# Performance work log

Hardware: AMD Instinct MI355X
Metric: run time of the kernel (lower is better)

Reference implementation:

```python
import jax, jax.numpy as jnp
import numpy as np

EPS = 1.1920929e-07  # torch nn.RMSNorm default eps = finfo(float32).eps
COS_EPS = 1e-8       # torch F.cosine_similarity denominator clamp

def rms_norm(x):
    # nn.RMSNorm(head_dim, elementwise_affine=False)
    return x / jnp.sqrt(jnp.mean(x * x, axis=-1, keepdims=True) + EPS)

def slerp(low, high, val):
    # spherical interpolation per last dim
    cos = jnp.sum(low * high, -1) / jnp.maximum(
        jnp.linalg.norm(low, axis=-1) * jnp.linalg.norm(high, axis=-1), COS_EPS)
    omega = jnp.arccos(jnp.clip(cos, -1.0 + 1e-7, 1.0 - 1e-7))[..., None]
    so = jnp.sin(omega)
    return (low * jnp.sin((1.0 - val) * omega) + high * jnp.sin(val * omega)) / so

def setup_inputs() -> dict:
    key = jax.random.key(0)
    k1, k2 = jax.random.split(key)
    z = jax.random.normal(k1, (8, 512, 2048), jnp.float32)          # [B, D, L]
    codebooks = rms_norm(jax.random.normal(k2, (8, 1024, 64), jnp.float32))  # [H, M, d]
    return {"z": z, "codebooks": codebooks}

def reference(z, codebooks, commitment_cost=0.25, decay=0.99):
    B, D, L = z.shape
    H, M, d = codebooks.shape
    # rearrange 'b (h d) l -> h (b l) d'
    z_split = z.reshape(B, H, d, L).transpose(1, 0, 3, 2).reshape(H, B * L, d)  # [H, N, d]

    sim = jnp.einsum('hnd,hmd->hnm', z_split, codebooks)          # [H, N, M]
    indices = jnp.argmax(sim, axis=-1)                            # [H, N]
    z_split_q = jnp.take_along_axis(codebooks, indices[:, :, None], axis=1)  # [H, N, d]

    commitment_loss = jnp.mean((jax.lax.stop_gradient(z_split) - z_split_q) ** 2)
    codebook_loss = jnp.mean((z_split - jax.lax.stop_gradient(z_split_q)) ** 2)
    vq_loss = codebook_loss + commitment_cost * commitment_loss

    # EMA slerp codebook update (training path, no_grad) -- vectorized over unique-code loop
    zs = jax.lax.stop_gradient(z_split)
    sums = jax.vmap(lambda zh, ih: jax.ops.segment_sum(zh, ih, num_segments=M))(zs, indices)  # [H, M, d]
    counts = jax.vmap(lambda ih: jax.ops.segment_sum(jnp.ones(ih.shape, zs.dtype), ih, num_segments=M))(indices)  # [H, M]
    means = sums / jnp.maximum(counts, 1.0)[..., None]
    updated = rms_norm(slerp(means, codebooks, decay))
    new_codebooks = jnp.where(counts[..., None] > 0, updated, codebooks)

    # rearrange back 'h (b l) d -> b (h d) l' and 'h (b l) -> b h l'
    z_q = z_split_q.reshape(H, B, L, d).transpose(1, 0, 3, 2).reshape(B, D, L)
    indices_out = indices.reshape(H, B, L).transpose(1, 0, 2)
    z_q = z + jax.lax.stop_gradient(z_q - z)  # straight-through
    return z_q, vq_loss, indices_out, new_codebooks
```

## Files before the change

kernel.cpp:

```cpp
#include <hip/hip_runtime.h>
#include <hip/hip_bf16.h>
#include <math.h>

#define BZ   8
#define DD   512
#define LL   2048
#define HH   8
#define MM   1024
#define DH   64
#define NN   (BZ * LL)
#define TOTAL_ELEMS (HH * NN * DH)

#define OFF_ZQ   0
#define OFF_LOSS 8388608
#define OFF_IDX  8388609
#define OFF_CB   8519681

#define CAP  128

#define WSB_SSE    0
#define WSB_CNT    64
#define WSB_LST    (64 + HH * MM * 4)
#define WSB_CBHI   (WSB_LST + HH * MM * CAP * 2)
#define WSB_CBLO   (WSB_CBHI + HH * MM * DH * 2)
#define WSB_ZS     (WSB_CBLO + HH * MM * DH * 2)
#define WS_NEED_BUCKET ((size_t)WSB_ZS + (size_t)HH * NN * DH * 4)

#define WS_PLANES_BYTE 64
#define WS_ZSPLIT_BYTE (64 + 2u * HH * MM * DH * 2)
#define WS_NEED_FAT    (WS_ZSPLIT_BYTE + (size_t)HH * NN * DH * 4)

typedef __attribute__((ext_vector_type(8))) short short8;
typedef __attribute__((ext_vector_type(4))) float float4v;

__device__ __forceinline__ unsigned short f2bf(float f) {
    unsigned int u = __builtin_bit_cast(unsigned int, f);
    u += 0x7FFFu + ((u >> 16) & 1u);
    return (unsigned short)(u >> 16);
}
__device__ __forceinline__ float bf2f(unsigned short s) {
    unsigned int u = ((unsigned int)s) << 16;
    return __builtin_bit_cast(float, u);
}

__device__ __forceinline__ void gload16(const short* g, short* l) {
    __builtin_amdgcn_global_load_lds(
        (const __attribute__((address_space(1))) unsigned int*)g,
        (__attribute__((address_space(3))) unsigned int*)l, 16, 0, 0);
}

__global__ __launch_bounds__(256) void cvt_cb_kernel(
    const float* __restrict__ cb, short* __restrict__ hip_, short* __restrict__ lop_)
{
    const int tid = blockIdx.x * 256 + threadIdx.x;
    const int c   = tid & 7;
    const int row = tid >> 3;
    const float* __restrict__ src = cb + (size_t)row * DH + c * 8;
    short hs[8], ls[8];
#pragma unroll
    for (int j = 0; j < 8; ++j) {
        const float f = src[j];
        const unsigned short hv = f2bf(f);
        hs[j] = (short)hv;
        ls[j] = (short)f2bf(f - bf2f(hv));
    }
    const int dst = row * DH + ((c ^ (row & 7)) * 8);
    *(short8*)&hip_[dst] = *(short8*)hs;
    *(short8*)&lop_[dst] = *(short8*)ls;
}

__global__ __launch_bounds__(512, 4) void vq_assign_kernel(
    const float* __restrict__ z,
    const float* __restrict__ cb,
    const short* __restrict__ cb_hi,
    const short* __restrict__ cb_lo,
    float* __restrict__ zq_out,
    float* __restrict__ idx_out,
    float* __restrict__ sse,
    float* __restrict__ zs,
    int*   __restrict__ cnts,
    unsigned short* __restrict__ lists)
{
    __shared__ __align__(16) short hi_lds[2][64 * DH];
    __shared__ __align__(16) short lo_lds[2][64 * DH];
    __shared__ float blk_err[8];

    const int t    = threadIdx.x;
    const int h    = blockIdx.y;
    const int lane = t & 63;
    const int g    = lane >> 4;
    const int nloc = lane & 15;
    const int w    = t >> 6;

    const int rbase = blockIdx.x * 256 + w * 32;

    short8 Bh0[2], Bh1[2], Bl0[2], Bl1[2];
#pragma unroll
    for (int u = 0; u < 2; ++u) {
        const int r = rbase + u * 16 + nloc;
        const int b = r >> 11;
        const int l = r & (LL - 1);
        const float* __restrict__ zbase = z + ((size_t)(b * DD + h * DH) * LL + l);
        float zv[16] __attribute__((aligned(16)));
#pragma unroll
        for (int j = 0; j < 8; ++j) zv[j]     = zbase[(size_t)(g * 8 + j) * LL];
#pragma unroll
        for (int j = 0; j < 8; ++j) zv[8 + j] = zbase[(size_t)(32 + g * 8 + j) * LL];

        if (zs) {
            float* __restrict__ zr_ = zs + ((size_t)h * NN + r) * DH;
            *(float4*)&zr_[g * 8]          = *(const float4*)&zv[0];
            *(float4*)&zr_[g * 8 + 4]      = *(const float4*)&zv[4];
            *(float4*)&zr_[32 + g * 8]     = *(const float4*)&zv[8];
            *(float4*)&zr_[32 + g * 8 + 4] = *(const float4*)&zv[12];
        }

        short bh[16], bl[16];
#pragma unroll
        for (int j = 0; j < 16; ++j) {
            const unsigned short hv = f2bf(zv[j]);
            bh[j] = (short)hv;
            bl[j] = (short)f2bf(zv[j] - bf2f(hv));
        }
        Bh0[u] = *(short8*)&bh[0];  Bh1[u] = *(short8*)&bh[8];
        Bl0[u] = *(short8*)&bl[0];  Bl1[u] = *(short8*)&bl[8];
    }

    const short* __restrict__ gh = cb_hi + (size_t)h * MM * DH;
    const short* __restrict__ gl = cb_lo + (size_t)h * MM * DH;

    auto stage = [&](int mt, int buf) {
        const short* sh = gh + (size_t)mt * 64 * DH;
        const short* sl = gl + (size_t)mt * 64 * DH;
        gload16(sh + t * 8, &hi_lds[buf][t * 8]);
        gload16(sl + t * 8, &lo_lds[buf][t * 8]);
    };

    stage(0, 0);

    float b1c[4], b2c[4];
    int   i1c[4], i2c[4];
#pragma unroll
    for (int c = 0; c < 4; ++c) { b1c[c] = -1e30f; b2c[c] = -1e30f; i1c[c] = 0; i2c[c] = 0; }

    const int sw8 = nloc & 7;

    for (int mt = 0; mt < MM / 64; ++mt) {
        __syncthreads();
        if (mt + 1 < MM / 64) stage(mt + 1, (mt + 1) & 1);
        const int buf = mt & 1;

#pragma unroll
        for (int s = 0; s < 4; ++s) {
            const short* hrow = &hi_lds[buf][(s * 16 + nloc) * DH];
            const short* lrow = &lo_lds[buf][(s * 16 + nloc) * DH];
            const short8 Ah0 = *(const short8*)&hrow[((g)     ^ sw8) * 8];
            const short8 Ah1 = *(const short8*)&hrow[((g + 4) ^ sw8) * 8];
            const short8 Al0 = *(const short8*)&lrow[((g)     ^ sw8) * 8];
            const short8 Al1 = *(const short8*)&lrow[((g + 4) ^ sw8) * 8];

            const int mbase = mt * 64 + s * 16 + g * 4;
#pragma unroll
            for (int u = 0; u < 2; ++u) {
                float4v acc = {0.f, 0.f, 0.f, 0.f};
                acc = __builtin_amdgcn_mfma_f32_16x16x32_bf16(Ah0, Bh0[u], acc, 0, 0, 0);
                acc = __builtin_amdgcn_mfma_f32_16x16x32_bf16(Ah1, Bh1[u], acc, 0, 0, 0);
                acc = __builtin_amdgcn_mfma_f32_16x16x32_bf16(Ah0, Bl0[u], acc, 0, 0, 0);
                acc = __builtin_amdgcn_mfma_f32_16x16x32_bf16(Ah1, Bl1[u], acc, 0, 0, 0);
                acc = __builtin_amdgcn_mfma_f32_16x16x32_bf16(Al0, Bh0[u], acc, 0, 0, 0);
                acc = __builtin_amdgcn_mfma_f32_16x16x32_bf16(Al1, Bh1[u], acc, 0, 0, 0);

#pragma unroll
                for (int reg = 0; reg < 4; ++reg) {
                    const int   c = u * 2 + (reg & 1);
                    const float v = acc[reg];
                    const int   m = mbase + reg;
                    const bool gt1 = v > b1c[c];
                    const bool gt2 = v > b2c[c];
                    b2c[c] = __builtin_amdgcn_fmed3f(v, b1c[c], b2c[c]);
                    i2c[c] = gt1 ? i1c[c] : (gt2 ? m : i2c[c]);
                    b1c[c] = fmaxf(v, b1c[c]);
                    i1c[c] = gt1 ? m : i1c[c];
                }
            }
        }
    }

    const float* __restrict__ cbh = cb + (size_t)h * MM * DH;
    float err_total = 0.f;

#pragma unroll
    for (int u = 0; u < 2; ++u) {
        float b1 = b1c[u * 2], b2 = b2c[u * 2];
        int   i1 = i1c[u * 2], i2 = i2c[u * 2];
        {
            const float ob1 = b1c[u * 2 + 1], ob2 = b2c[u * 2 + 1];
            const int   oi1 = i1c[u * 2 + 1], oi2 = i2c[u * 2 + 1];
            const bool agt = (b1 > ob1) || (b1 == ob1 && i1 < oi1);
            const float w1 = agt ? b1 : ob1;  const int wi1 = agt ? i1 : oi1;
            const float l1 = agt ? ob1 : b1;  const int li1 = agt ? oi1 : i1;
            const float w2 = agt ? b2 : ob2;  const int wi2 = agt ? i2 : oi2;
            const bool sgt = (l1 > w2) || (l1 == w2 && li1 < wi2);
            b1 = w1;  i1 = wi1;
            b2 = sgt ? l1 : w2;  i2 = sgt ? li1 : wi2;
        }

#pragma unroll
        for (int off = 16; off <= 32; off <<= 1) {
            float ob1 = __shfl_xor(b1, off, 64);
            int   oi1 = __shfl_xor(i1, off, 64);
            float ob2 = __shfl_xor(b2, off, 64);
            int   oi2 = __shfl_xor(i2, off, 64);
            const bool agt = (b1 > ob1) || (b1 == ob1 && i1 < oi1);
            const float w1  = agt ? b1 : ob1;  const int wi1 = agt ? i1 : oi1;
            const float l1  = agt ? ob1 : b1;  const int li1 = agt ? oi1 : i1;
            const float w2  = agt ? b2 : ob2;  const int wi2 = agt ? i2 : oi2;
            const bool sgt = (l1 > w2) || (l1 == w2 && li1 < wi2);
            b1 = w1;  i1 = wi1;
            b2 = sgt ? l1 : w2;  i2 = sgt ? li1 : wi2;
        }

        const int r = rbase + u * 16 + nloc;
        const int b = r >> 11;
        const int l = r & (LL - 1);

        float zr[16] __attribute__((aligned(16)));
        if (zs) {
            const float* __restrict__ zp = zs + ((size_t)h * NN + r) * DH;
            *(float4*)&zr[0]  = *(const float4*)&zp[g * 8];
            *(float4*)&zr[4]  = *(const float4*)&zp[g * 8 + 4];
            *(float4*)&zr[8]  = *(const float4*)&zp[32 + g * 8];
            *(float4*)&zr[12] = *(const float4*)&zp[32 + g * 8 + 4];
        } else {
            const float* __restrict__ zbase = z + ((size_t)(b * DD + h * DH) * LL + l);
#pragma unroll
            for (int j = 0; j < 8; ++j) zr[j]     = zbase[(size_t)(g * 8 + j) * LL];
#pragma unroll
            for (int j = 0; j < 8; ++j) zr[8 + j] = zbase[(size_t)(32 + g * 8 + j) * LL];
        }

        const float* __restrict__ c1 = cbh + (size_t)i1 * DH;
        const float* __restrict__ c2 = cbh + (size_t)i2 * DH;
        double d1 = 0.0, d2 = 0.0;
#pragma unroll
        for (int j = 0; j < 8; ++j) {
            const int k0 = g * 8 + j, k1 = 32 + g * 8 + j;
            d1 = fma((double)zr[j],     (double)c1[k0], d1);
            d1 = fma((double)zr[8 + j], (double)c1[k1], d1);
            d2 = fma((double)zr[j],     (double)c2[k0], d2);
            d2 = fma((double)zr[8 + j], (double)c2[k1], d2);
        }
        d1 += __shfl_xor(d1, 16, 64);  d1 += __shfl_xor(d1, 32, 64);
        d2 += __shfl_xor(d2, 16, 64);  d2 += __shfl_xor(d2, 32, 64);
        const int best = (d2 > d1 || (d2 == d1 && i2 < i1)) ? i2 : i1;

        const float* __restrict__ cq = cbh + (size_t)best * DH;
        float* __restrict__ zqp = zq_out + ((size_t)(b * DD + h * DH) * LL + l);
        float err = 0.f;
#pragma unroll
        for (int j = 0; j < 8; ++j) {
            const int k0 = g * 8 + j, k1 = 32 + g * 8 + j;
            const float q0 = cq[k0], q1 = cq[k1];
            zqp[(size_t)k0 * LL] = q0;
            zqp[(size_t)k1 * LL] = q1;
            const float e0 = zr[j] - q0, e1 = zr[8 + j] - q1;
            err = fmaf(e0, e0, err);
            err = fmaf(e1, e1, err);
        }
        if (g == 0) {
            idx_out[((size_t)b * HH + h) * LL + l] = (float)best;
            if (cnts) {
                const int code = h * MM + best;
                const int slot = atomicAdd(&cnts[code], 1);
                if (slot < CAP) lists[(size_t)code * CAP + slot] = (unsigned short)r;
            }
        }
        err_total += err;
    }

#pragma unroll
    for (int off = 32; off; off >>= 1) err_total += __shfl_xor(err_total, off, 64);
    if (lane == 0) blk_err[w] = err_total;
    __syncthreads();
    if (t == 0) {
        float s = 0.f;
#pragma unroll
        for (int i = 0; i < 8; ++i) s += blk_err[i];
        atomicAdd(sse, s);
    }
}

__global__ __launch_bounds__(256) void vq_update_kernel(
    const float* __restrict__ z,
    const float* __restrict__ zs,
    const float* __restrict__ cb,
    const float* __restrict__ idx,
    const float* __restrict__ sse,
    float* __restrict__ cb_out,
    float* __restrict__ loss_out,
    const int* __restrict__ cnts,
    const unsigned short* __restrict__ lists)
{
    if (blockIdx.x == 0 && threadIdx.x == 0) {
        loss_out[0] = 1.25f * sse[0] / (float)TOTAL_ELEMS;
    }
    const int row  = blockIdx.x * 4 + (threadIdx.x >> 6);
    const int lane = threadIdx.x & 63;
    const int h    = row >> 10;
    const int m    = row & (MM - 1);
    const float fm = (float)m;

    float acc = 0.f;
    int   cnt = 0;
    bool  fast = false;
    if (cnts) { cnt = cnts[row]; fast = (cnt <= CAP); }

    if (fast) {
        const unsigned short* __restrict__ lst = lists + (size_t)row * CAP;
        const float* __restrict__ zsh = zs + ((size_t)h * NN) * DH + lane;
        float a0 = 0.f, a1 = 0.f, a2 = 0.f, a3 = 0.f;
        int i = 0;
        for (; i + 4 <= cnt; i += 4) {
            const int n0 = lst[i], n1 = lst[i + 1], n2 = lst[i + 2], n3 = lst[i + 3];
            a0 += zsh[(size_t)n0 * DH];
            a1 += zsh[(size_t)n1 * DH];
            a2 += zsh[(size_t)n2 * DH];
            a3 += zsh[(size_t)n3 * DH];
        }
        for (; i < cnt; ++i) acc += zsh[(size_t)lst[i] * DH];
        acc += (a0 + a1) + (a2 + a3);
    } else {
        cnt = 0;
#pragma unroll 1
        for (int b = 0; b < BZ; ++b) {
            const float* __restrict__ ip  = idx + ((size_t)(b * HH + h)) * LL;
            const float* __restrict__ zb  = z + ((size_t)(b * DD + h * DH + lane)) * LL;
            const float* __restrict__ zsb = zs ? (zs + ((size_t)h * NN + (size_t)b * LL) * DH + lane)
                                              : (const float*)0;
            float4 cur = *(const float4*)(ip + lane * 4);
#pragma unroll 1
            for (int it = 0; it < LL / 256; ++it) {
                float4 nxt = cur;
                if (it + 1 < LL / 256)
                    nxt = *(const float4*)(ip + (it + 1) * 256 + lane * 4);
#pragma unroll
                for (int j = 0; j < 4; ++j) {
                    const float ivj = (&cur.x)[j];
                    unsigned long long mask = __ballot(ivj == fm);
                    cnt += (int)__popcll(mask);
                    while (mask) {
                        const int src = (int)__ffsll((long long)mask) - 1;
                        mask &= mask - 1;
                        const int l = it * 256 + src * 4 + j;
                        acc += zsb ? zsb[(size_t)l * DH]
                                   : zb[l];
                    }
                }
                cur = nxt;
            }
        }
    }

    const float cf   = (float)cnt;
    const float c    = cb[(size_t)row * DH + lane];
    const float mean = acc / fmaxf(cf, 1.0f);

    float dot = mean * c;
    float nl  = mean * mean;
    float nh  = c * c;
#pragma unroll
    for (int off = 32; off; off >>= 1) {
        dot += __shfl_xor(dot, off, 64);
        nl  += __shfl_xor(nl,  off, 64);
        nh  += __shfl_xor(nh,  off, 64);
    }

    float cosv = dot / fmaxf(sqrtf(nl) * sqrtf(nh), 1e-8f);
    cosv = fminf(fmaxf(cosv, -0.9999999f), 0.9999999f);
    const float omega = acosf(cosv);
    const float so    = sinf(omega);
    float outv = (mean * sinf(0.01f * omega) + c * sinf(0.99f * omega)) / so;

    float ms = outv * outv;
#pragma unroll
    for (int off = 32; off; off >>= 1) ms += __shfl_xor(ms, off, 64);
    ms = ms * (1.0f / (float)DH) + 1.1920929e-07f;
    const float normed = outv / sqrtf(ms);

    cb_out[(size_t)row * DH + lane] = (cnt > 0) ? normed : c;
}

extern "C" void kernel_launch(void* const* d_in, const int* in_sizes, int n_in,
                              void* d_out, int out_size, void* d_ws, size_t ws_size,
                              hipStream_t stream) {
    const float* z  = (const float*)d_in[0];
    const float* cb = (const float*)d_in[1];
    float* out = (float*)d_out;

    const bool bucket = ws_size >= WS_NEED_BUCKET;
    const bool fat    = ws_size >= WS_NEED_FAT;

    short *cb_hi, *cb_lo;
    float *zs = 0;
    int   *cnts = 0;
    unsigned short *lists = 0;

    if (bucket) {
        cnts  = (int*)((char*)d_ws + WSB_CNT);
        lists = (unsigned short*)((char*)d_ws + WSB_LST);
        cb_hi = (short*)((char*)d_ws + WSB_CBHI);
        cb_lo = (short*)((char*)d_ws + WSB_CBLO);
        zs    = (float*)((char*)d_ws + WSB_ZS);
        hipMemsetAsync(d_ws, 0, WSB_LST, stream);
    } else {
        cb_hi = (short*)((char*)d_ws + WS_PLANES_BYTE);
        cb_lo = cb_hi + (size_t)HH * MM * DH;
        zs    = fat ? (float*)((char*)d_ws + WS_ZSPLIT_BYTE) : (float*)0;
        hipMemsetAsync(d_ws, 0, 64, stream);
    }

    cvt_cb_kernel<<<(HH * MM * DH / 8) / 256, 256, 0, stream>>>(cb, cb_hi, cb_lo);

    dim3 gridA(NN / 256, HH);
    vq_assign_kernel<<<gridA, 512, 0, stream>>>(
        z, cb, cb_hi, cb_lo,
        out + OFF_ZQ, out + OFF_IDX, (float*)d_ws, zs, cnts, lists);

    dim3 gridB((HH * MM) / 4);
    vq_update_kernel<<<gridB, 256, 0, stream>>>(
        z, zs, cb, out + OFF_IDX, (float*)d_ws,
        out + OFF_CB, out + OFF_LOSS, cnts, lists);
}
```

Measured before the change: 195.3 us.

## Fuse codebook conversion, assignment and update into one persistent kernel with grid barriers

Combines the bf16 split conversion, the assignment and the EMA update into one kernel launched with 512 blocks, separated by atomic-counter grid barriers. Count zeroing moves into the kernel so the large memset shrinks to 64 bytes. The aim is to remove two kernel launch gaps and the big memset. It relies on all 512 blocks being co-resident (4 per CU via launch bounds) and the spin barriers add sync cost; the update phase now runs at 512-thread granularity with two codes per wave.

```diff
diff --git a/kernel.cpp b/kernel.cpp
--- a/kernel.cpp
+++ b/kernel.cpp
@@ -49,10 +49,22 @@
         (__attribute__((address_space(3))) unsigned int*)l, 16, 0, 0);
 }
 
-__global__ __launch_bounds__(256) void cvt_cb_kernel(
-    const float* __restrict__ cb, short* __restrict__ hip_, short* __restrict__ lop_)
-{
-    const int tid = blockIdx.x * 256 + threadIdx.x;
+__device__ __forceinline__ void grid_sync(unsigned int* done, unsigned int target) {
+    __threadfence();
+    __syncthreads();
+    if (threadIdx.x == 0) {
+        __hip_atomic_fetch_add(done, 1u, __ATOMIC_ACQ_REL, __HIP_MEMORY_SCOPE_AGENT);
+        while (__hip_atomic_load(done, __ATOMIC_ACQUIRE, __HIP_MEMORY_SCOPE_AGENT) < target) {
+            __builtin_amdgcn_s_sleep(8);
+        }
+    }
+    __syncthreads();
+    __threadfence();
+}
+
+__device__ __forceinline__ void cvt_task(int tid, const float* __restrict__ cb,
+                                         short* __restrict__ hip_, short* __restrict__ lop_)
+{
     const int c   = tid & 7;
     const int row = tid >> 3;
     const float* __restrict__ src = cb + (size_t)row * DH + c * 8;
@@ -69,7 +81,13 @@
     *(short8*)&lop_[dst] = *(short8*)ls;
 }
 
-__global__ __launch_bounds__(512, 4) void vq_assign_kernel(
+__global__ __launch_bounds__(256) void cvt_cb_kernel(
+    const float* __restrict__ cb, short* __restrict__ hip_, short* __restrict__ lop_)
+{
+    cvt_task(blockIdx.x * 256 + threadIdx.x, cb, hip_, lop_);
+}
+
+__device__ __forceinline__ void assign_phase(
     const float* __restrict__ z,
     const float* __restrict__ cb,
     const short* __restrict__ cb_hi,
@@ -79,20 +97,17 @@
     float* __restrict__ sse,
     float* __restrict__ zs,
     int*   __restrict__ cnts,
-    unsigned short* __restrict__ lists)
-{
-    __shared__ __align__(16) short hi_lds[2][64 * DH];
-    __shared__ __align__(16) short lo_lds[2][64 * DH];
-    __shared__ float blk_err[8];
-
+    unsigned short* __restrict__ lists,
+    short (*hi_lds)[64 * DH], short (*lo_lds)[64 * DH], float* blk_err,
+    int bx, int h)
+{
     const int t    = threadIdx.x;
-    const int h    = blockIdx.y;
     const int lane = t & 63;
     const int g    = lane >> 4;
     const int nloc = lane & 15;
     const int w    = t >> 6;
 
-    const int rbase = blockIdx.x * 256 + w * 32;
+    const int rbase = bx * 256 + w * 32;
 
     short8 Bh0[2], Bh1[2], Bl0[2], Bl1[2];
 #pragma unroll
@@ -290,24 +305,18 @@
     }
 }
 
-__global__ __launch_bounds__(256) void vq_update_kernel(
+__device__ __forceinline__ void update_code(
+    int row, int lane,
     const float* __restrict__ z,
     const float* __restrict__ zs,
     const float* __restrict__ cb,
     const float* __restrict__ idx,
-    const float* __restrict__ sse,
     float* __restrict__ cb_out,
-    float* __restrict__ loss_out,
     const int* __restrict__ cnts,
     const unsigned short* __restrict__ lists)
 {
-    if (blockIdx.x == 0 && threadIdx.x == 0) {
-        loss_out[0] = 1.25f * sse[0] / (float)TOTAL_ELEMS;
-    }
-    const int row  = blockIdx.x * 4 + (threadIdx.x >> 6);
-    const int lane = threadIdx.x & 63;
-    const int h    = row >> 10;
-    const int m    = row & (MM - 1);
+    const int h = row >> 10;
+    const int m = row & (MM - 1);
     const float fm = (float)m;
 
     float acc = 0.f;
@@ -390,6 +399,77 @@
     cb_out[(size_t)row * DH + lane] = (cnt > 0) ? normed : c;
 }
 
+__global__ __launch_bounds__(512, 4) void vq_fused_kernel(
+    const float* __restrict__ z,
+    const float* __restrict__ cb,
+    short* __restrict__ cb_hi,
+    short* __restrict__ cb_lo,
+    float* __restrict__ zq_out,
+    float* __restrict__ idx_out,
+    float* __restrict__ sse,
+    float* __restrict__ zs,
+    int*   __restrict__ cnts,
+    unsigned short* __restrict__ lists,
+    float* __restrict__ cb_out,
+    float* __restrict__ loss_out,
+    unsigned int* __restrict__ done)
+{
+    __shared__ __align__(16) short hi_lds[2][64 * DH];
+    __shared__ __align__(16) short lo_lds[2][64 * DH];
+    __shared__ float blk_err[8];
+
+    const int bid  = blockIdx.y * gridDim.x + blockIdx.x;
+    const unsigned int nblk = gridDim.x * gridDim.y;
+
+    {
+        const int tid = bid * 512 + threadIdx.x;
+        if (tid < HH * MM * DH / 8) cvt_task(tid, cb, cb_hi, cb_lo);
+        if (tid < HH * MM) cnts[tid] = 0;
+    }
+    grid_sync(done, nblk);
+
+    assign_phase(z, cb, cb_hi, cb_lo, zq_out, idx_out, sse, zs, cnts, lists,
+                 hi_lds, lo_lds, blk_err, blockIdx.x, blockIdx.y);
+    grid_sync(done, 2 * nblk);
+
+    if (bid == 0 && threadIdx.x == 0)
+        loss_out[0] = 1.25f * sse[0] / (float)TOTAL_ELEMS;
+    const int w    = threadIdx.x >> 6;
+    const int lane = threadIdx.x & 63;
+    const int wid  = bid * 8 + w;
+    update_code(wid,        lane, z, zs, cb, idx_out, cb_out, cnts, lists);
+    update_code(wid + 4096, lane, z, zs, cb, idx_out, cb_out, cnts, lists);
+}
+
+__global__ __launch_bounds__(512, 4) void vq_assign_kernel(
+    const float* __restrict__ z, const float* __restrict__ cb,
+    const short* __restrict__ cb_hi, const short* __restrict__ cb_lo,
+    float* __restrict__ zq_out, float* __restrict__ idx_out,
+    float* __restrict__ sse, float* __restrict__ zs,
+    int* __restrict__ cnts, unsigned short* __restrict__ lists)
+{
+    __shared__ __align__(16) short hi_lds[2][64 * DH];
+    __shared__ __align__(16) short lo_lds[2][64 * DH];
+    __shared__ float blk_err[8];
+    assign_phase(z, cb, cb_hi, cb_lo, zq_out, idx_out, sse, zs, cnts, lists,
+                 hi_lds, lo_lds, blk_err, blockIdx.x, blockIdx.y);
+}
+
+__global__ __launch_bounds__(256) void vq_update_kernel(
+    const float* __restrict__ z, const float* __restrict__ zs,
+    const float* __restrict__ cb, const float* __restrict__ idx,
+    const float* __restrict__ sse, float* __restrict__ cb_out,
+    float* __restrict__ loss_out,
+    const int* __restrict__ cnts, const unsigned short* __restrict__ lists)
+{
+    if (blockIdx.x == 0 && threadIdx.x == 0) {
+        loss_out[0] = 1.25f * sse[0] / (float)TOTAL_ELEMS;
+    }
+    const int row  = blockIdx.x * 4 + (threadIdx.x >> 6);
+    const int lane = threadIdx.x & 63;
+    update_code(row, lane, z, zs, cb, idx, cb_out, cnts, lists);
+}
+
 extern "C" void kernel_launch(void* const* d_in, const int* in_sizes, int n_in,
                               void* d_out, int out_size, void* d_ws, size_t ws_size,
                               hipStream_t stream) {
@@ -400,34 +480,37 @@
     const bool bucket = ws_size >= WS_NEED_BUCKET;
     const bool fat    = ws_size >= WS_NEED_FAT;
 
-    short *cb_hi, *cb_lo;
-    float *zs = 0;
-    int   *cnts = 0;
-    unsigned short *lists = 0;
-
     if (bucket) {
-        cnts  = (int*)((char*)d_ws + WSB_CNT);
-        lists = (unsigned short*)((char*)d_ws + WSB_LST);
-        cb_hi = (short*)((char*)d_ws + WSB_CBHI);
-        cb_lo = (short*)((char*)d_ws + WSB_CBLO);
-        zs    = (float*)((char*)d_ws + WSB_ZS);
-        hipMemsetAsync(d_ws, 0, WSB_LST, stream);
+        int* cnts             = (int*)((char*)d_ws + WSB_CNT);
+        unsigned short* lists = (unsigned short*)((char*)d_ws + WSB_LST);
+        short* cb_hi          = (short*)((char*)d_ws + WSB_CBHI);
+        short* cb_lo          = (short*)((char*)d_ws + WSB_CBLO);
+        float* zs             = (float*)((char*)d_ws + WSB_ZS);
+        unsigned int* done    = (unsigned int*)((char*)d_ws + 16);
+
+        hipMemsetAsync(d_ws, 0, 64, stream);
+
+        vq_fused_kernel<<<dim3(NN / 256, HH), 512, 0, stream>>>(
+            z, cb, cb_hi, cb_lo,
+            out + OFF_ZQ, out + OFF_IDX, (float*)d_ws, zs, cnts, lists,
+            out + OFF_CB, out + OFF_LOSS, done);
     } else {
-        cb_hi = (short*)((char*)d_ws + WS_PLANES_BYTE);
-        cb_lo = cb_hi + (size_t)HH * MM * DH;
-        zs    = fat ? (float*)((char*)d_ws + WS_ZSPLIT_BYTE) : (float*)0;
+        short* cb_hi = (short*)((char*)d_ws + WS_PLANES_BYTE);
+        short* cb_lo = cb_hi + (size_t)HH * MM * DH;
+        float* zs    = fat ? (float*)((char*)d_ws + WS_ZSPLIT_BYTE) : (float*)0;
+
         hipMemsetAsync(d_ws, 0, 64, stream);
-    }
-
-    cvt_cb_kernel<<<(HH * MM * DH / 8) / 256, 256, 0, stream>>>(cb, cb_hi, cb_lo);
-
-    dim3 gridA(NN / 256, HH);
-    vq_assign_kernel<<<gridA, 512, 0, stream>>>(
-        z, cb, cb_hi, cb_lo,
-        out + OFF_ZQ, out + OFF_IDX, (float*)d_ws, zs, cnts, lists);
-
-    dim3 gridB((HH * MM) / 4);
-    vq_update_kernel<<<gridB, 256, 0, stream>>>(
-        z, zs, cb, out + OFF_IDX, (float*)d_ws,
-        out + OFF_CB, out + OFF_LOSS, cnts, lists);
-}
+
+        cvt_cb_kernel<<<(HH * MM * DH / 8) / 256, 256, 0, stream>>>(cb, cb_hi, cb_lo);
+
+        dim3 gridA(NN / 256, HH);
+        vq_assign_kernel<<<gridA, 512, 0, stream>>>(
+            z, cb, cb_hi, cb_lo,
+            out + OFF_ZQ, out + OFF_IDX, (float*)d_ws, zs, (int*)0, (unsigned short*)0);
+
+        dim3 gridB((HH * MM) / 4);
+        vq_update_kernel<<<gridB, 256, 0, stream>>>(
+            z, zs, cb, out + OFF_IDX, (float*)d_ws,
+            out + OFF_CB, out + OFF_LOSS, (int*)0, (unsigned short*)0);
+    }
+}
```

Result: slower. 647.9 us (+231.8%).
